# Performance work log

Hardware: AMD Instinct MI355X
Metric: run time of the kernel (lower is better)

The kernel has to match this reference:

```python
import jax, jax.numpy as jnp
import numpy as np

H, W = 480, 640
N, Q, K = 128, 8192, 10
MIN_DEPTH = 0.1


def setup_inputs() -> dict:
    key = jax.random.key(0)
    ks = jax.random.split(key, 8)
    pred_depth = jax.random.uniform(ks[0], (1, H, W), jnp.float32, 0.5, 10.0)
    gt_depth = jax.random.uniform(ks[1], (1, H, W), jnp.float32, 0.0, 10.0)
    gt_masks = jax.random.uniform(ks[2], (N, H, W)) > 0.5
    random_mask = jax.random.uniform(ks[3], (N, H, W)) > 0.95  # matches torch.rand>0.95
    k_matrix = jnp.array([[500.0, 0.0, W / 2.0], [0.0, 500.0, H / 2.0], [0.0, 0.0, 1.0]], jnp.float32)
    xq = jax.random.randint(ks[4], (N, Q), 0, H, jnp.int32)
    yq = jax.random.randint(ks[5], (N, Q), 0, W, jnp.int32)
    xp = jax.random.randint(ks[6], (N, K), 0, H, jnp.int32)
    yp = jax.random.randint(ks[7], (N, K), 0, W, jnp.int32)
    return {"pred_depth": pred_depth, "gt_masks": gt_masks, "gt_depth": gt_depth,
            "k_matrix": k_matrix, "random_mask": random_mask,
            "xq": xq, "yq": yq, "xp": xp, "yp": yp}


def reference(pred_depth, gt_masks, gt_depth, k_matrix, random_mask, xq, yq, xp, yp):
    sg = jax.lax.stop_gradient
    d0 = pred_depth[0]  # [H, W]
    fx, fy = k_matrix[0, 0], k_matrix[1, 1]
    u0 = jnp.float32(W // 2)
    v0 = jnp.float32(H // 2)
    u_u0 = jnp.arange(W, dtype=jnp.float32)[None, :] - u0  # [1, W]
    v_v0 = jnp.arange(H, dtype=jnp.float32)[:, None] - v0  # [H, 1]
    # point cloud pw: [H, W, 3]
    px_map = u_u0 * jnp.abs(d0) / fx
    py_map = v_v0 * jnp.abs(d0) / fy
    pw = jnp.stack([px_map, py_map, d0], axis=-1)

    # candidate weights per mask: gt_mask & (rand>0.95) & (gt_depth > min_depth)
    valid = gt_depth[0] > MIN_DEPTH  # [H, W]
    w = (gt_masks & random_mask & valid[None]).astype(jnp.float32)  # [N, H, W]

    # weighted least-squares plane fit z = a*x + b*y + d  (normal equations, same as (A^T A)^-1 A^T b)
    feat = jnp.stack([px_map, py_map, jnp.ones_like(d0)], axis=-1)  # [H, W, 3]
    M = jnp.einsum('nhw,hwi,hwj->nij', w, feat, feat)  # [N, 3, 3]
    rhs = jnp.einsum('nhw,hwi,hw->ni', w, feat, d0)    # [N, 3]
    cnt = w.sum(axis=(1, 2))
    ok = (jnp.abs(jnp.linalg.det(M)) > 1e-8) & (cnt >= 3.0)  # emulate try/except skip
    M_safe = jnp.where(ok[:, None, None], M, jnp.eye(3, dtype=M.dtype))
    fit = sg(jnp.linalg.solve(M_safe, rhs[..., None])[..., 0])  # [N, 3]; detached (numpy in original)
    a, b, d = fit[:, 0:1], fit[:, 1:2], fit[:, 2:3]

    # gather query / propagated point coordinates (detached in original)
    qx = sg(pw[xq, yq, 0])  # [N, Q]
    qy = sg(pw[xq, yq, 1])
    ppx = sg(pw[xp, yp, 0])  # [N, K]
    ppy = sg(pw[xp, yp, 1])
    pd = d0[xp, yp]          # [N, K], grads flow through these depths

    num = a * qx + b * qy + d   # [N, Q]
    den = a * ppx + b * ppy + d  # [N, K]
    vals = num * jnp.mean(pd / den, axis=1, keepdims=True)  # [N, Q]

    # sequential scatter per mask (later masks overwrite earlier, as in the loop)
    def step(out, t):
        xi, yi, vi, oki = t
        cur = out[xi, yi]
        out = out.at[xi, yi].set(jnp.where(oki, vi, cur))
        return out, None

    out, _ = jax.lax.scan(step, d0, (xq, yq, vals, ok))
    return out[None]
```

## Files before the change

kernel.cpp:

```cpp
#include <hip/hip_runtime.h>

#define H_ 480
#define W_ 640
#define HW 307200
#define NN 128
#define QQ 8192
#define KK 10
#define G_ 6
#define PIXB 6144

#define WS_FLAG   0
#define WS_ACC    64
#define WS_ABD    8192
#define WS_VBITS  16384
#define WS_PRIO   65536
#define WS_PACK   1294336
#define WS_NEED   (WS_PACK + (size_t)NN * 38400)

typedef unsigned int u32x4 __attribute__((ext_vector_type(4)));

__global__ __launch_bounds__(256) void prep_k(const unsigned int* __restrict__ gm,
                                              const float* __restrict__ gtd,
                                              unsigned long long* __restrict__ vbits,
                                              int* __restrict__ prio,
                                              float* __restrict__ acc,
                                              int* __restrict__ flag)
{
    const int pix = blockIdx.x * 256 + threadIdx.x;
    prio[pix] = 0;
    if (pix < NN * 12) acc[pix] = 0.0f;
    const bool v = gtd[pix] > 0.1f;
    const unsigned long long b = __ballot(v);
    if ((threadIdx.x & 63) == 0) vbits[pix >> 6] = b;

    if (blockIdx.x == 0) {
        __shared__ int sf;
        if (threadIdx.x == 0) sf = 0;
        __syncthreads();
        int f = 0;
        for (int i = threadIdx.x; i < 4096; i += 256) {
            const unsigned int w = gm[i];
            if (w == 0x3F800000u) f |= 2;
            else if (w > 1u) f |= 1;
        }
        if (f) atomicOr(&sf, f);
        __syncthreads();
        if (threadIdx.x == 0) *flag = (sf & 2) ? 2 : ((sf & 1) ? 1 : 0);
    }
}

__device__ __forceinline__ unsigned nib4v(const u32x4 a, const u32x4 b)
{
    return ((a.x & b.x) ? 1u : 0u) | ((a.y & b.y) ? 2u : 0u)
         | ((a.z & b.z) ? 4u : 0u) | ((a.w & b.w) ? 8u : 0u);
}

__device__ __forceinline__ unsigned nib4(const uint4& a, const uint4& b)
{
    return ((a.x & b.x) ? 1u : 0u) | ((a.y & b.y) ? 2u : 0u)
         | ((a.z & b.z) ? 4u : 0u) | ((a.w & b.w) ? 8u : 0u);
}

__global__ __launch_bounds__(256) void compress_k(
    const void* __restrict__ gmv,
    const void* __restrict__ rmv,
    const int* __restrict__ flag,
    const unsigned long long* __restrict__ vbits,
    unsigned char* __restrict__ packed)
{
    const int fmt = *flag;
    const unsigned char* __restrict__ vb8 = (const unsigned char*)vbits;
    const int tid0 = blockIdx.x * 256 + (int)threadIdx.x;
    const int stride = 2048 * 256;
    const unsigned lane = threadIdx.x & 63u;

    if (fmt != 1) {
        const u32x4* __restrict__ gp = (const u32x4*)gmv;
        const u32x4* __restrict__ rp = (const u32x4*)rmv;
        for (int i = tid0; i < NN * HW / 4; i += stride) {
            const u32x4 a = __builtin_nontemporal_load(gp + i);
            const u32x4 b = __builtin_nontemporal_load(rp + i);
            const unsigned m = nib4v(a, b);
            const unsigned hi = __shfl_down(m, 1);
            if (!(lane & 1u)) {
                const int g = i >> 1;
                packed[g] = (unsigned char)((m | (hi << 4)) & vb8[g % 38400]);
            }
        }
    } else {
        const unsigned long long* __restrict__ gp = (const unsigned long long*)gmv;
        const unsigned long long* __restrict__ rp = (const unsigned long long*)rmv;
        for (int g = tid0; g < NN * HW / 8; g += stride) {
            const unsigned long long ab = __builtin_nontemporal_load(gp + g)
                                        & __builtin_nontemporal_load(rp + g);
            unsigned m = 0;
            #pragma unroll
            for (int j = 0; j < 8; ++j)
                m |= (unsigned)(((ab >> (8*j)) & 0xFFull) != 0) << j;
            packed[g] = (unsigned char)(m & vb8[g % 38400]);
        }
    }
}

__global__ __launch_bounds__(192) void reduce2_k(
    const float* __restrict__ d0,
    const unsigned long long* __restrict__ packed,
    const float* __restrict__ km,
    float* __restrict__ acc)
{
    const int n = blockIdx.y;
    const int w = blockIdx.x * 192 + (int)threadIdx.x;
    unsigned long long bits = packed[(size_t)n * 4800 + w];
    const float rfx = 1.0f / km[0], rfy = 1.0f / km[4];

    float s0=0.f,s1=0.f,s2=0.f,s3=0.f,s4=0.f,s5=0.f,s6=0.f,s7=0.f,s8=0.f;
    if (bits) {
        const int r = w / 10;
        const int c0 = (w - r * 10) * 64;
        const float pyb = (float)(r - 240) * rfy;
        const float* drow = d0 + r * W_ + c0;
        while (bits) {
            const int j = __ffsll((unsigned long long)bits) - 1;
            bits &= bits - 1;
            const float d = drow[j];
            const float ad = fabsf(d);
            const float px = (float)(c0 + j - 320) * ad * rfx;
            const float py = pyb * ad;
            s0 += px*px; s1 += px*py; s2 += px;
            s3 += py*py; s4 += py;    s5 += 1.0f;
            s6 += px*d;  s7 += py*d;  s8 += d;
        }
    }

    float s[9] = {s0,s1,s2,s3,s4,s5,s6,s7,s8};
    #pragma unroll
    for (int off = 32; off > 0; off >>= 1) {
        #pragma unroll
        for (int i = 0; i < 9; ++i) s[i] += __shfl_down(s[i], off);
    }
    __shared__ float ls[3][9];
    const int wave = threadIdx.x >> 6, lane = threadIdx.x & 63;
    if (lane == 0) {
        #pragma unroll
        for (int i = 0; i < 9; ++i) ls[wave][i] = s[i];
    }
    __syncthreads();
    if (threadIdx.x < 9) {
        const int i = threadIdx.x;
        atomicAdd(&acc[n*12 + i], ls[0][i] + ls[1][i] + ls[2][i]);
    }
}

__global__ __launch_bounds__(256) void reduce_k(
    const float* __restrict__ d0,
    const void* __restrict__ gmv,
    const void* __restrict__ rmv,
    const float* __restrict__ km,
    const int* __restrict__ flag,
    const unsigned long long* __restrict__ vbits,
    float* __restrict__ acc)
{
    const int n = blockIdx.y;
    const int base = blockIdx.x * PIXB + (int)threadIdx.x * 4;
    const int fmt = *flag;
    const float rfx = 1.0f / km[0], rfy = 1.0f / km[4];
    const size_t moff = (size_t)n * HW;

    unsigned bitsArr[G_];
    if (fmt != 1) {
        uint4 ga[G_], ra[G_];
        #pragma unroll
        for (int g = 0; g < G_; ++g) {
            const int p = base + g * 1024;
            ga[g] = *reinterpret_cast<const uint4*>((const unsigned*)gmv + moff + p);
            ra[g] = *reinterpret_cast<const uint4*>((const unsigned*)rmv + moff + p);
        }
        #pragma unroll
        for (int g = 0; g < G_; ++g) bitsArr[g] = nib4(ga[g], ra[g]);
    } else {
        unsigned ga[G_], ra[G_];
        #pragma unroll
        for (int g = 0; g < G_; ++g) {
            const int p = base + g * 1024;
            ga[g] = *reinterpret_cast<const unsigned*>((const unsigned char*)gmv + moff + p);
            ra[g] = *reinterpret_cast<const unsigned*>((const unsigned char*)rmv + moff + p);
        }
        #pragma unroll
        for (int g = 0; g < G_; ++g) {
            const unsigned ab = ga[g] & ra[g];
            bitsArr[g] = (unsigned)((ab & 0xFFu) != 0) | ((unsigned)(((ab>>8) & 0xFFu) != 0) << 1)
                       | ((unsigned)(((ab>>16) & 0xFFu) != 0) << 2) | ((unsigned)((ab>>24) != 0) << 3);
        }
    }

    float s0=0.f,s1=0.f,s2=0.f,s3=0.f,s4=0.f,s5=0.f,s6=0.f,s7=0.f,s8=0.f;
    #pragma unroll
    for (int g = 0; g < G_; ++g) {
        const int p0 = base + g * 1024;
        unsigned bits = bitsArr[g] & ((unsigned)(vbits[p0 >> 6] >> (p0 & 63)) & 0xFu);
        if (bits) {
            const float4 dv = *reinterpret_cast<const float4*>(d0 + p0);
            const int r = p0 / W_;
            const int c0 = p0 - r * W_;
            const float pyb = (float)(r - 240) * rfy;
            while (bits) {
                const int j = __ffs(bits) - 1;
                bits &= bits - 1;
                const float d = (j == 0) ? dv.x : (j == 1) ? dv.y : (j == 2) ? dv.z : dv.w;
                const float ad = fabsf(d);
                const float px = (float)(c0 + j - 320) * ad * rfx;
                const float py = pyb * ad;
                s0 += px*px; s1 += px*py; s2 += px;
                s3 += py*py; s4 += py;    s5 += 1.0f;
                s6 += px*d;  s7 += py*d;  s8 += d;
            }
        }
    }

    float s[9] = {s0,s1,s2,s3,s4,s5,s6,s7,s8};
    #pragma unroll
    for (int off = 32; off > 0; off >>= 1) {
        #pragma unroll
        for (int i = 0; i < 9; ++i) s[i] += __shfl_down(s[i], off);
    }
    __shared__ float ls[4][9];
    const int wave = threadIdx.x >> 6, lane = threadIdx.x & 63;
    if (lane == 0) {
        #pragma unroll
        for (int i = 0; i < 9; ++i) ls[wave][i] = s[i];
    }
    __syncthreads();
    if (threadIdx.x == 0) {
        #pragma unroll
        for (int i = 0; i < 9; ++i)
            atomicAdd(&acc[n*12 + i], ls[0][i] + ls[1][i] + ls[2][i] + ls[3][i]);
    }
}

__global__ void solve_k(const float* __restrict__ acc,
                        const float* __restrict__ d0,
                        const float* __restrict__ km,
                        const int* __restrict__ xp,
                        const int* __restrict__ yp,
                        float* __restrict__ abd)
{
    const int n = blockIdx.x * blockDim.x + threadIdx.x;
    if (n >= NN) return;
    const float* s = acc + n * 12;
    const double M00=s[0], M01=s[1], M02=s[2], M11=s[3], M12=s[4], M22=s[5];
    const double r0=s[6], r1=s[7], r2=s[8];
    const double cnt = M22;
    const double c00 = M11*M22 - M12*M12;
    const double c01 = M01*M22 - M12*M02;
    const double c02 = M01*M12 - M11*M02;
    const double det = M00*c00 - M01*c01 + M02*c02;
    const bool ok = (fabs(det) > 1e-8) && (cnt >= 3.0);
    float a = 0.f, b = 0.f, dc = 0.f, scale = 0.f;
    if (ok) {
        const double inv = 1.0 / det;
        const double t1 = r1*M22 - r2*M12;
        const double t2 = M01*r2 - r1*M02;
        const double x0 = (r0*c00 - M01*t1 + M02*(r1*M12 - r2*M11)) * inv;
        const double x1 = (M00*t1 - r0*c01 + M02*t2) * inv;
        const double x2 = (M00*(M11*r2 - r1*M12) - M01*t2 + r0*c02) * inv;
        a = (float)x0; b = (float)x1; dc = (float)x2;
        const float fx = km[0], fy = km[4];
        float sum = 0.0f;
        for (int k = 0; k < KK; ++k) {
            const int xi = xp[n*KK + k], yi = yp[n*KK + k];
            const float dd = d0[xi * W_ + yi];
            const float ad = fabsf(dd);
            const float ppx = (float)(yi - 320) * ad / fx;
            const float ppy = (float)(xi - 240) * ad / fy;
            const float den = a * ppx + b * ppy + dc;
            sum += dd / den;
        }
        scale = sum / (float)KK;
    }
    abd[n*8+0] = a; abd[n*8+1] = b; abd[n*8+2] = dc;
    abd[n*8+3] = scale;
    abd[n*8+4] = ok ? 1.0f : 0.0f;
}

__global__ __launch_bounds__(256) void prio_k(const int* __restrict__ xq,
                                              const int* __restrict__ yq,
                                              const float* __restrict__ abd,
                                              int* __restrict__ prio)
{
    const int idx = (blockIdx.x * 256 + threadIdx.x) * 4;
    const int n = idx >> 13;
    if (abd[n*8+4] == 0.0f) return;
    const int4 xs = *reinterpret_cast<const int4*>(xq + idx);
    const int4 ys = *reinterpret_cast<const int4*>(yq + idx);
    const int np = n + 1;
    atomicMax(prio + xs.x * W_ + ys.x, np);
    atomicMax(prio + xs.y * W_ + ys.y, np);
    atomicMax(prio + xs.z * W_ + ys.z, np);
    atomicMax(prio + xs.w * W_ + ys.w, np);
}

__global__ __launch_bounds__(256) void final_k(const int* __restrict__ prio,
                                               const float* __restrict__ abd,
                                               const float* __restrict__ d0,
                                               const float* __restrict__ km,
                                               float* __restrict__ out)
{
    const int p0 = (blockIdx.x * 256 + threadIdx.x) * 4;
    const int4 pr4 = *reinterpret_cast<const int4*>(prio + p0);
    const float4 dv = *reinterpret_cast<const float4*>(d0 + p0);
    const float rfx = 1.0f / km[0], rfy = 1.0f / km[4];
    const int r = p0 / W_;
    const int c0 = p0 - r * W_;
    const float yv = (float)(r - 240) * rfy;
    const int pr[4] = {pr4.x, pr4.y, pr4.z, pr4.w};
    const float dd[4] = {dv.x, dv.y, dv.z, dv.w};
    float o[4];
    #pragma unroll
    for (int j = 0; j < 4; ++j) {
        float v = dd[j];
        if (pr[j] > 0) {
            const int n = pr[j] - 1;
            const float ad = fabsf(dd[j]);
            const float qx = (float)(c0 + j - 320) * ad * rfx;
            const float qy = yv * ad;
            v = (abd[n*8+0]*qx + abd[n*8+1]*qy + abd[n*8+2]) * abd[n*8+3];
        }
        o[j] = v;
    }
    *reinterpret_cast<float4*>(out + p0) = make_float4(o[0], o[1], o[2], o[3]);
}

extern "C" void kernel_launch(void* const* d_in, const int* in_sizes, int n_in,
                              void* d_out, int out_size, void* d_ws, size_t ws_size,
                              hipStream_t stream)
{
    const float* d0  = (const float*)d_in[0];
    const void*  gm  = d_in[1];
    const float* gtd = (const float*)d_in[2];
    const float* km  = (const float*)d_in[3];
    const void*  rm  = d_in[4];
    const int*   xq  = (const int*)d_in[5];
    const int*   yq  = (const int*)d_in[6];
    const int*   xp  = (const int*)d_in[7];
    const int*   yp  = (const int*)d_in[8];
    float* out = (float*)d_out;
    char*  ws  = (char*)d_ws;

    int* flag = (int*)(ws + WS_FLAG);
    float* acc = (float*)(ws + WS_ACC);
    float* abd = (float*)(ws + WS_ABD);
    unsigned long long* vbits = (unsigned long long*)(ws + WS_VBITS);
    int* prio = (int*)(ws + WS_PRIO);
    unsigned char* packed = (unsigned char*)(ws + WS_PACK);

    prep_k<<<HW / 256, 256, 0, stream>>>((const unsigned int*)gm, gtd, vbits, prio, acc, flag);
    if (ws_size >= WS_NEED) {
        compress_k<<<2048, 256, 0, stream>>>(gm, rm, flag, vbits, packed);
        reduce2_k<<<dim3(25, NN), 192, 0, stream>>>(d0, (const unsigned long long*)packed, km, acc);
    } else {
        reduce_k<<<dim3(HW / PIXB, NN), 256, 0, stream>>>(d0, gm, rm, km, flag, vbits, acc);
    }
    solve_k<<<2, 64, 0, stream>>>(acc, d0, km, xp, yp, abd);
    prio_k<<<(NN * QQ / 4) / 256, 256, 0, stream>>>(xq, yq, abd, prio);
    final_k<<<(HW / 4) / 256, 256, 0, stream>>>(prio, abd, d0, km, out);
}
```

Before: 119.9 us.

## Write byte-per-nibble packed masks and move valid-bit masking into reduce

```diff
diff --git a/kernel.cpp b/kernel.cpp
--- a/kernel.cpp
+++ b/kernel.cpp
@@ -15,7 +15,9 @@
 #define WS_VBITS  16384
 #define WS_PRIO   65536
 #define WS_PACK   1294336
-#define WS_NEED   (WS_PACK + (size_t)NN * 38400)
+#define WS_NEED   (WS_PACK + (size_t)NN * 76800)
+
+#define CB 2400
 
 typedef unsigned int u32x4 __attribute__((ext_vector_type(4)));
 
@@ -65,53 +67,59 @@
     const void* __restrict__ gmv,
     const void* __restrict__ rmv,
     const int* __restrict__ flag,
-    const unsigned long long* __restrict__ vbits,
     unsigned char* __restrict__ packed)
 {
     const int fmt = *flag;
-    const unsigned char* __restrict__ vb8 = (const unsigned char*)vbits;
-    const int tid0 = blockIdx.x * 256 + (int)threadIdx.x;
-    const int stride = 2048 * 256;
-    const unsigned lane = threadIdx.x & 63u;
+    const int t0 = blockIdx.x * 256 + (int)threadIdx.x;
+    const int stride = CB * 256;
 
     if (fmt != 1) {
         const u32x4* __restrict__ gp = (const u32x4*)gmv;
         const u32x4* __restrict__ rp = (const u32x4*)rmv;
-        for (int i = tid0; i < NN * HW / 4; i += stride) {
+        #pragma unroll 4
+        for (int k = 0; k < 16; ++k) {
+            const int i = t0 + k * stride;
             const u32x4 a = __builtin_nontemporal_load(gp + i);
             const u32x4 b = __builtin_nontemporal_load(rp + i);
-            const unsigned m = nib4v(a, b);
-            const unsigned hi = __shfl_down(m, 1);
-            if (!(lane & 1u)) {
-                const int g = i >> 1;
-                packed[g] = (unsigned char)((m | (hi << 4)) & vb8[g % 38400]);
-            }
+            packed[i] = (unsigned char)nib4v(a, b);
         }
     } else {
-        const unsigned long long* __restrict__ gp = (const unsigned long long*)gmv;
-        const unsigned long long* __restrict__ rp = (const unsigned long long*)rmv;
-        for (int g = tid0; g < NN * HW / 8; g += stride) {
-            const unsigned long long ab = __builtin_nontemporal_load(gp + g)
-                                        & __builtin_nontemporal_load(rp + g);
-            unsigned m = 0;
-            #pragma unroll
-            for (int j = 0; j < 8; ++j)
-                m |= (unsigned)(((ab >> (8*j)) & 0xFFull) != 0) << j;
-            packed[g] = (unsigned char)(m & vb8[g % 38400]);
+        const unsigned* __restrict__ gp = (const unsigned*)gmv;
+        const unsigned* __restrict__ rp = (const unsigned*)rmv;
+        #pragma unroll 4
+        for (int k = 0; k < 16; ++k) {
+            const int i = t0 + k * stride;
+            const unsigned ab = __builtin_nontemporal_load(gp + i)
+                              & __builtin_nontemporal_load(rp + i);
+            const unsigned m = (unsigned)((ab & 0xFFu) != 0)
+                             | ((unsigned)(((ab >> 8) & 0xFFu) != 0) << 1)
+                             | ((unsigned)(((ab >> 16) & 0xFFu) != 0) << 2)
+                             | ((unsigned)((ab >> 24) != 0) << 3);
+            packed[i] = (unsigned char)m;
         }
     }
 }
 
 __global__ __launch_bounds__(192) void reduce2_k(
     const float* __restrict__ d0,
-    const unsigned long long* __restrict__ packed,
+    const unsigned char* __restrict__ packed,
+    const unsigned long long* __restrict__ vbits,
     const float* __restrict__ km,
     float* __restrict__ acc)
 {
     const int n = blockIdx.y;
     const int w = blockIdx.x * 192 + (int)threadIdx.x;
-    unsigned long long bits = packed[(size_t)n * 4800 + w];
+    const uint4 pk = *reinterpret_cast<const uint4*>(packed + (size_t)n * 76800 + w * 16);
     const float rfx = 1.0f / km[0], rfy = 1.0f / km[4];
+
+    unsigned t0 = pk.x; t0 = (t0 | (t0 >> 4)) & 0x00FF00FFu; t0 = (t0 | (t0 >> 8)) & 0xFFFFu;
+    unsigned t1 = pk.y; t1 = (t1 | (t1 >> 4)) & 0x00FF00FFu; t1 = (t1 | (t1 >> 8)) & 0xFFFFu;
+    unsigned t2 = pk.z; t2 = (t2 | (t2 >> 4)) & 0x00FF00FFu; t2 = (t2 | (t2 >> 8)) & 0xFFFFu;
+    unsigned t3 = pk.w; t3 = (t3 | (t3 >> 4)) & 0x00FF00FFu; t3 = (t3 | (t3 >> 8)) & 0xFFFFu;
+    unsigned long long bits =
+        (unsigned long long)t0 | ((unsigned long long)t1 << 16)
+      | ((unsigned long long)t2 << 32) | ((unsigned long long)t3 << 48);
+    bits &= vbits[w];
 
     float s0=0.f,s1=0.f,s2=0.f,s3=0.f,s4=0.f,s5=0.f,s6=0.f,s7=0.f,s8=0.f;
     if (bits) {
@@ -355,8 +363,8 @@
 
     prep_k<<<HW / 256, 256, 0, stream>>>((const unsigned int*)gm, gtd, vbits, prio, acc, flag);
     if (ws_size >= WS_NEED) {
-        compress_k<<<2048, 256, 0, stream>>>(gm, rm, flag, vbits, packed);
-        reduce2_k<<<dim3(25, NN), 192, 0, stream>>>(d0, (const unsigned long long*)packed, km, acc);
+        compress_k<<<CB, 256, 0, stream>>>(gm, rm, flag, packed);
+        reduce2_k<<<dim3(25, NN), 192, 0, stream>>>(d0, packed, vbits, km, acc);
     } else {
         reduce_k<<<dim3(HW / PIXB, NN), 256, 0, stream>>>(d0, gm, rm, km, flag, vbits, acc);
     }
```

New measurement: 128.8 us. 1.07x slower.
